# Performance work log

Measured on AMD Instinct MI355X. Metric: run time of the kernel, lower is better.

Reference implementation:

```python
import jax, jax.numpy as jnp
import numpy as np

B, N = 128, 128
FEAT_IN = 6   # feature_dim(4) + class + score
E = 32        # embedding_dim
NUM_CLASSES = 80


def setup_inputs() -> dict:
    key = jax.random.key(0)
    ks = jax.random.split(key, 20)
    def glorot(k, shape):
        fan_in, fan_out = shape[0], shape[1]
        lim = jnp.sqrt(6.0 / (fan_in + fan_out)).astype(jnp.float32)
        return jax.random.uniform(k, shape, jnp.float32, -lim, lim)
    return {
        'boxes': jax.random.uniform(ks[0], (B, N, 4), jnp.float32),
        'classes': jax.random.randint(ks[1], (B, N), 0, NUM_CLASSES),
        'scores': jax.random.uniform(ks[2], (B, N), jnp.float32),
        'num_objects': jax.random.randint(ks[3], (B,), 1, N + 1),
        # feature_encoder: Linear(6->32), ReLU, Linear(32->32)
        'W1': glorot(ks[4], (FEAT_IN, E)), 'b1': jnp.zeros((E,), jnp.float32),
        'W2': glorot(ks[5], (E, E)),       'b2': jnp.zeros((E,), jnp.float32),
        # isObject: Linear(32->32), ReLU, Linear(32->1), Sigmoid
        'Wo1': glorot(ks[6], (E, E)),  'bo1': jnp.zeros((E,), jnp.float32),
        'Wo2': glorot(ks[7], (E, 1)),  'bo2': jnp.zeros((1,), jnp.float32),
        # sameClass: Linear(64->32), ReLU, Linear(32->1), Sigmoid
        'Ws1': glorot(ks[8], (2 * E, E)), 'bs1': jnp.zeros((E,), jnp.float32),
        'Ws2': glorot(ks[9], (E, 1)),     'bs2': jnp.zeros((1,), jnp.float32),
    }


def reference(boxes, classes, scores, num_objects, W1, b1, W2, b2,
              Wo1, bo1, Wo2, bo2, Ws1, bs1, Ws2, bs2):
    # encode: [B,N,6] -> [B,N,E]
    combined = jnp.concatenate(
        [boxes, classes.astype(jnp.float32)[..., None], scores[..., None]], axis=-1)
    enc = jax.nn.relu(combined @ W1 + b1) @ W2 + b2                 # [B,N,E]

    # isObject predicate -> [B,N]
    isobj = jax.nn.sigmoid(jax.nn.relu(enc @ Wo1 + bo1) @ Wo2 + bo2)[..., 0]

    # sameClass on all pairs: split concat-weight so we never build [B,N,N,2E]
    Wsx, Wsy = Ws1[:E], Ws1[E:]
    hx = enc @ Wsx                                                  # [B,N,E]
    hy = enc @ Wsy                                                  # [B,N,E]
    h = jax.nn.relu(hx[:, :, None, :] + hy[:, None, :, :] + bs1)    # [B,N,N,E]
    same = jax.nn.sigmoid(h @ Ws2 + bs2)[..., 0]                    # [B,N,N] (x,y)

    # inner = And_min(isObject(y), sameClass(x,y))
    inner = jnp.minimum(isobj[:, None, :], same)                    # [B,N,N]

    mask = jnp.arange(N)[None, :] < num_objects[:, None]            # [B,N] valid objs
    n = num_objects.astype(jnp.float32)
    denom = jnp.maximum(n, 1.0)

    # Exists_y = mean over valid y
    exists = jnp.sum(inner * mask[:, None, :], axis=-1) / denom[:, None]  # [B,N]

    # outer = Or_max(Not(isObject(x)), exists)
    outer = jnp.maximum(1.0 - isobj, exists)                        # [B,N]

    # Forall_x = min over valid x (pad with 1.0, never the min for valid batches)
    sat_b = jnp.min(jnp.where(mask, outer, 1.0), axis=-1)           # [B]

    valid = (num_objects > 0).astype(jnp.float32)
    cnt = jnp.sum(valid)
    total = jnp.where(cnt > 0,
                      jnp.sum(sat_b * valid) / jnp.maximum(cnt, 1.0),
                      jnp.float32(1.0))
    return total
```

## Files before the change

### kernel.cpp

```cpp
#include <hip/hip_runtime.h>

#define BB 128
#define NN 128
#define EE 32


__global__ __launch_bounds__(256) void ltn_fused(
    const float* __restrict__ boxes, const int* __restrict__ classes,
    const float* __restrict__ scores, const int* __restrict__ num_objects,
    const float* __restrict__ W1, const float* __restrict__ b1,
    const float* __restrict__ W2, const float* __restrict__ b2,
    const float* __restrict__ Wo1, const float* __restrict__ bo1,
    const float* __restrict__ Wo2, const float* __restrict__ bo2,
    const float* __restrict__ Ws1, const float* __restrict__ bs1,
    const float* __restrict__ Ws2, const float* __restrict__ bs2,
    float* __restrict__ ws)
{
    __shared__ float hyS[128 * 36];
    __shared__ float hxS[128 * 36];
    __shared__ float rows[16 * 36];
    __shared__ float isoS[128];
    __shared__ float wred[4];

    const int t = threadIdx.x;
    const int b = blockIdx.x >> 1;
    const int half = blockIdx.x & 1;
    const int e = t & 31;
    const int g = t >> 5;

    float w1c[6];
#pragma unroll
    for (int f = 0; f < 6; f++) w1c[f] = W1[f * 32 + e];
    float w2c[32], wo1c[32], wsxc[32], wsyc[32];
#pragma unroll
    for (int k = 0; k < 32; k++) {
        w2c[k]  = W2[k * 32 + e];
        wo1c[k] = Wo1[k * 32 + e];
        wsxc[k] = Ws1[k * 32 + e];
        wsyc[k] = Ws1[(32 + k) * 32 + e];
    }
    const float b1e  = b1[e];
    const float b2e  = b2[e];
    const float bo1e = bo1[e];
    const float wo2e = Wo2[e];
    const float bo2s = bo2[0];

    const int il0 = g * 16;
#pragma unroll 2
    for (int it = 0; it < 16; ++it) {
        const int il = il0 + it;
        const int item = b * 128 + il;
        float* row = rows + (g * 2 + (it & 1)) * 36;

        const float4 bx = ((const float4*)boxes)[item];
        const float c4 = (float)classes[item];
        const float c5 = scores[item];

        float h1 = b1e;
        h1 = fmaf(bx.x, w1c[0], h1);
        h1 = fmaf(bx.y, w1c[1], h1);
        h1 = fmaf(bx.z, w1c[2], h1);
        h1 = fmaf(bx.w, w1c[3], h1);
        h1 = fmaf(c4,   w1c[4], h1);
        h1 = fmaf(c5,   w1c[5], h1);
        h1 = fmaxf(h1, 0.f);

        row[e] = h1;

        float a0 = 0.f, a1 = 0.f, a2 = 0.f, a3 = 0.f;
#pragma unroll
        for (int kk = 0; kk < 8; kk++) {
            const float4 h = *(const float4*)(row + kk * 4);
            a0 = fmaf(h.x, w2c[4 * kk + 0], a0);
            a1 = fmaf(h.y, w2c[4 * kk + 1], a1);
            a2 = fmaf(h.z, w2c[4 * kk + 2], a2);
            a3 = fmaf(h.w, w2c[4 * kk + 3], a3);
        }
        const float enc = ((a0 + a1) + (a2 + a3)) + b2e;
        row[e] = enc;

        float u = bo1e, hx = 0.f, hy = 0.f;
#pragma unroll
        for (int kk = 0; kk < 8; kk++) {
            const float4 ec = *(const float4*)(row + kk * 4);
            const int k0 = 4 * kk;
            u  = fmaf(ec.x, wo1c[k0 + 0], u);
            u  = fmaf(ec.y, wo1c[k0 + 1], u);
            u  = fmaf(ec.z, wo1c[k0 + 2], u);
            u  = fmaf(ec.w, wo1c[k0 + 3], u);
            hx = fmaf(ec.x, wsxc[k0 + 0], hx);
            hx = fmaf(ec.y, wsxc[k0 + 1], hx);
            hx = fmaf(ec.z, wsxc[k0 + 2], hx);
            hx = fmaf(ec.w, wsxc[k0 + 3], hx);
            hy = fmaf(ec.x, wsyc[k0 + 0], hy);
            hy = fmaf(ec.y, wsyc[k0 + 1], hy);
            hy = fmaf(ec.z, wsyc[k0 + 2], hy);
            hy = fmaf(ec.w, wsyc[k0 + 3], hy);
        }
        u = fmaxf(u, 0.f);

        float v = u * wo2e;
        v += __shfl_xor(v, 16, 32);
        v += __shfl_xor(v, 8, 32);
        v += __shfl_xor(v, 4, 32);
        v += __shfl_xor(v, 2, 32);
        v += __shfl_xor(v, 1, 32);

        hyS[il * 36 + e] = hy;
        hxS[il * 36 + e] = hx;
        if (e == 0)
            isoS[il] = 1.f / (1.f + __expf(-(v + bo2s)));
    }
    __syncthreads();

    const int nb = num_objects[b];
    const int p  = t >> 3;
    const int li0 = half * 64 + p * 2;
    const int li1 = li0 + 1;
    const int s  = t & 7;

    float hxb0[32], hxb1[32];
#pragma unroll
    for (int kk = 0; kk < 8; kk++) {
        const float4 a = ((const float4*)(hxS + li0 * 36))[kk];
        const float4 c = ((const float4*)(hxS + li1 * 36))[kk];
        const int k0 = 4 * kk;
        hxb0[k0 + 0] = a.x + bs1[k0 + 0];  hxb1[k0 + 0] = c.x + bs1[k0 + 0];
        hxb0[k0 + 1] = a.y + bs1[k0 + 1];  hxb1[k0 + 1] = c.y + bs1[k0 + 1];
        hxb0[k0 + 2] = a.z + bs1[k0 + 2];  hxb1[k0 + 2] = c.z + bs1[k0 + 2];
        hxb0[k0 + 3] = a.w + bs1[k0 + 3];  hxb1[k0 + 3] = c.w + bs1[k0 + 3];
    }
    float w2[32];
#pragma unroll
    for (int k = 0; k < 32; k++) w2[k] = Ws2[k];
    const float bbias = bs2[0];

    float acc0 = 0.f, acc1 = 0.f;
    for (int j = s; j < nb; j += 8) {
        const float4* hr4 = (const float4*)(hyS + j * 36);
        float d0 = bbias, d1 = 0.f, d2 = 0.f, d3 = 0.f;
        float e0 = bbias, e1 = 0.f, e2 = 0.f, e3 = 0.f;
#pragma unroll
        for (int kk = 0; kk < 8; kk++) {
            const float4 h = hr4[kk];
            const int k0 = 4 * kk;
            d0 = fmaf(fmaxf(hxb0[k0 + 0] + h.x, 0.f), w2[k0 + 0], d0);
            d1 = fmaf(fmaxf(hxb0[k0 + 1] + h.y, 0.f), w2[k0 + 1], d1);
            d2 = fmaf(fmaxf(hxb0[k0 + 2] + h.z, 0.f), w2[k0 + 2], d2);
            d3 = fmaf(fmaxf(hxb0[k0 + 3] + h.w, 0.f), w2[k0 + 3], d3);
            e0 = fmaf(fmaxf(hxb1[k0 + 0] + h.x, 0.f), w2[k0 + 0], e0);
            e1 = fmaf(fmaxf(hxb1[k0 + 1] + h.y, 0.f), w2[k0 + 1], e1);
            e2 = fmaf(fmaxf(hxb1[k0 + 2] + h.z, 0.f), w2[k0 + 2], e2);
            e3 = fmaf(fmaxf(hxb1[k0 + 3] + h.w, 0.f), w2[k0 + 3], e3);
        }
        const float dd = (d0 + d1) + (d2 + d3);
        const float ee = (e0 + e1) + (e2 + e3);
        const float same0 = 1.f / (1.f + __expf(-dd));
        const float same1 = 1.f / (1.f + __expf(-ee));
        const float iso_j = isoS[j];
        acc0 += fminf(iso_j, same0);
        acc1 += fminf(iso_j, same1);
    }
    acc0 += __shfl_xor(acc0, 1);  acc1 += __shfl_xor(acc1, 1);
    acc0 += __shfl_xor(acc0, 2);  acc1 += __shfl_xor(acc1, 2);
    acc0 += __shfl_xor(acc0, 4);  acc1 += __shfl_xor(acc1, 4);

    const float denom = (float)(nb > 1 ? nb : 1);
    const float ex0 = acc0 / denom;
    const float ex1 = acc1 / denom;
    const float o0 = fmaxf(1.f - isoS[li0], ex0);
    const float o1 = fmaxf(1.f - isoS[li1], ex1);
    float val = fminf((li0 < nb) ? o0 : 1.f, (li1 < nb) ? o1 : 1.f);

    val = fminf(val, __shfl_xor(val, 8));
    val = fminf(val, __shfl_xor(val, 16));
    val = fminf(val, __shfl_xor(val, 32));
    if ((t & 63) == 0) wred[t >> 6] = val;
    __syncthreads();

    if (t == 0)
        ws[blockIdx.x] = fminf(fminf(wred[0], wred[1]), fminf(wred[2], wred[3]));
}

__global__ __launch_bounds__(128) void finalize_kernel(
    const int* __restrict__ num_objects, const float* __restrict__ ws,
    float* __restrict__ out)
{
    __shared__ float r1[2], r2[2];
    const int t = threadIdx.x;
    const float sat = fminf(ws[2 * t], ws[2 * t + 1]);
    const float valid = (num_objects[t] > 0) ? 1.f : 0.f;
    float contrib = sat * valid;
    float vcnt = valid;
#pragma unroll
    for (int off = 1; off < 64; off <<= 1) {
        contrib += __shfl_xor(contrib, off);
        vcnt    += __shfl_xor(vcnt, off);
    }
    if ((t & 63) == 0) { r1[t >> 6] = contrib; r2[t >> 6] = vcnt; }
    __syncthreads();
    if (t == 0) {
        const float sc = r1[0] + r1[1];
        const float cn = r2[0] + r2[1];
        out[0] = (cn > 0.f) ? (sc / cn) : 1.f;
    }
}

extern "C" void kernel_launch(void* const* d_in, const int* in_sizes, int n_in,
                              void* d_out, int out_size, void* d_ws, size_t ws_size,
                              hipStream_t stream)
{
    const float* boxes       = (const float*)d_in[0];
    const int*   classes     = (const int*)d_in[1];
    const float* scores      = (const float*)d_in[2];
    const int*   num_objects = (const int*)d_in[3];
    const float* W1  = (const float*)d_in[4];
    const float* b1  = (const float*)d_in[5];
    const float* W2  = (const float*)d_in[6];
    const float* b2  = (const float*)d_in[7];
    const float* Wo1 = (const float*)d_in[8];
    const float* bo1 = (const float*)d_in[9];
    const float* Wo2 = (const float*)d_in[10];
    const float* bo2 = (const float*)d_in[11];
    const float* Ws1 = (const float*)d_in[12];
    const float* bs1 = (const float*)d_in[13];
    const float* Ws2 = (const float*)d_in[14];
    const float* bs2 = (const float*)d_in[15];

    float* ws  = (float*)d_ws;
    float* out = (float*)d_out;

    ltn_fused<<<256, 256, 0, stream>>>(boxes, classes, scores, num_objects,
                                       W1, b1, W2, b2, Wo1, bo1, Wo2, bo2,
                                       Ws1, bs1, Ws2, bs2, ws);
    finalize_kernel<<<1, 128, 0, stream>>>(num_objects, ws, out);
}
```

Before: 104.4 us.

## Double block size to 512 threads, one x-row per thread group

Launches 512 threads per block instead of 256. The encoder stage now gives each 32-lane group 8 items instead of 16, and the pairwise stage gives each 8-thread group a single x row instead of two. This doubles the resident threads per block to hide latency and shortens the per-thread serial work. In exchange, each hy row loaded from shared memory is reused for only one x row, and the per-thread register budget is tighter under the 512-thread launch bound, because every thread still keeps about 128 weight values in registers.

```diff
diff --git a/kernel.cpp b/kernel.cpp
--- a/kernel.cpp
+++ b/kernel.cpp
@@ -5,7 +5,7 @@
 #define EE 32
 
 
-__global__ __launch_bounds__(256) void ltn_fused(
+__global__ __launch_bounds__(512) void ltn_fused(
     const float* __restrict__ boxes, const int* __restrict__ classes,
     const float* __restrict__ scores, const int* __restrict__ num_objects,
     const float* __restrict__ W1, const float* __restrict__ b1,
@@ -18,9 +18,9 @@
 {
     __shared__ float hyS[128 * 36];
     __shared__ float hxS[128 * 36];
-    __shared__ float rows[16 * 36];
+    __shared__ float rows[32 * 36];
     __shared__ float isoS[128];
-    __shared__ float wred[4];
+    __shared__ float wred[8];
 
     const int t = threadIdx.x;
     const int b = blockIdx.x >> 1;
@@ -45,9 +45,9 @@
     const float wo2e = Wo2[e];
     const float bo2s = bo2[0];
 
-    const int il0 = g * 16;
+    const int il0 = g * 8;
 #pragma unroll 2
-    for (int it = 0; it < 16; ++it) {
+    for (int it = 0; it < 8; ++it) {
         const int il = il0 + it;
         const int item = b * 128 + il;
         float* row = rows + (g * 2 + (it & 1)) * 36;
@@ -115,62 +115,49 @@
 
     const int nb = num_objects[b];
     const int p  = t >> 3;
-    const int li0 = half * 64 + p * 2;
-    const int li1 = li0 + 1;
+    const int li = half * 64 + p;
     const int s  = t & 7;
 
-    float hxb0[32], hxb1[32];
+    float hxb[32];
 #pragma unroll
     for (int kk = 0; kk < 8; kk++) {
-        const float4 a = ((const float4*)(hxS + li0 * 36))[kk];
-        const float4 c = ((const float4*)(hxS + li1 * 36))[kk];
+        const float4 a = ((const float4*)(hxS + li * 36))[kk];
         const int k0 = 4 * kk;
-        hxb0[k0 + 0] = a.x + bs1[k0 + 0];  hxb1[k0 + 0] = c.x + bs1[k0 + 0];
-        hxb0[k0 + 1] = a.y + bs1[k0 + 1];  hxb1[k0 + 1] = c.y + bs1[k0 + 1];
-        hxb0[k0 + 2] = a.z + bs1[k0 + 2];  hxb1[k0 + 2] = c.z + bs1[k0 + 2];
-        hxb0[k0 + 3] = a.w + bs1[k0 + 3];  hxb1[k0 + 3] = c.w + bs1[k0 + 3];
+        hxb[k0 + 0] = a.x + bs1[k0 + 0];
+        hxb[k0 + 1] = a.y + bs1[k0 + 1];
+        hxb[k0 + 2] = a.z + bs1[k0 + 2];
+        hxb[k0 + 3] = a.w + bs1[k0 + 3];
     }
     float w2[32];
 #pragma unroll
     for (int k = 0; k < 32; k++) w2[k] = Ws2[k];
     const float bbias = bs2[0];
 
-    float acc0 = 0.f, acc1 = 0.f;
+    float acc = 0.f;
     for (int j = s; j < nb; j += 8) {
         const float4* hr4 = (const float4*)(hyS + j * 36);
         float d0 = bbias, d1 = 0.f, d2 = 0.f, d3 = 0.f;
-        float e0 = bbias, e1 = 0.f, e2 = 0.f, e3 = 0.f;
 #pragma unroll
         for (int kk = 0; kk < 8; kk++) {
             const float4 h = hr4[kk];
             const int k0 = 4 * kk;
-            d0 = fmaf(fmaxf(hxb0[k0 + 0] + h.x, 0.f), w2[k0 + 0], d0);
-            d1 = fmaf(fmaxf(hxb0[k0 + 1] + h.y, 0.f), w2[k0 + 1], d1);
-            d2 = fmaf(fmaxf(hxb0[k0 + 2] + h.z, 0.f), w2[k0 + 2], d2);
-            d3 = fmaf(fmaxf(hxb0[k0 + 3] + h.w, 0.f), w2[k0 + 3], d3);
-            e0 = fmaf(fmaxf(hxb1[k0 + 0] + h.x, 0.f), w2[k0 + 0], e0);
-            e1 = fmaf(fmaxf(hxb1[k0 + 1] + h.y, 0.f), w2[k0 + 1], e1);
-            e2 = fmaf(fmaxf(hxb1[k0 + 2] + h.z, 0.f), w2[k0 + 2], e2);
-            e3 = fmaf(fmaxf(hxb1[k0 + 3] + h.w, 0.f), w2[k0 + 3], e3);
+            d0 = fmaf(fmaxf(hxb[k0 + 0] + h.x, 0.f), w2[k0 + 0], d0);
+            d1 = fmaf(fmaxf(hxb[k0 + 1] + h.y, 0.f), w2[k0 + 1], d1);
+            d2 = fmaf(fmaxf(hxb[k0 + 2] + h.z, 0.f), w2[k0 + 2], d2);
+            d3 = fmaf(fmaxf(hxb[k0 + 3] + h.w, 0.f), w2[k0 + 3], d3);
         }
         const float dd = (d0 + d1) + (d2 + d3);
-        const float ee = (e0 + e1) + (e2 + e3);
-        const float same0 = 1.f / (1.f + __expf(-dd));
-        const float same1 = 1.f / (1.f + __expf(-ee));
-        const float iso_j = isoS[j];
-        acc0 += fminf(iso_j, same0);
-        acc1 += fminf(iso_j, same1);
-    }
-    acc0 += __shfl_xor(acc0, 1);  acc1 += __shfl_xor(acc1, 1);
-    acc0 += __shfl_xor(acc0, 2);  acc1 += __shfl_xor(acc1, 2);
-    acc0 += __shfl_xor(acc0, 4);  acc1 += __shfl_xor(acc1, 4);
+        const float same = 1.f / (1.f + __expf(-dd));
+        acc += fminf(isoS[j], same);
+    }
+    acc += __shfl_xor(acc, 1);
+    acc += __shfl_xor(acc, 2);
+    acc += __shfl_xor(acc, 4);
 
     const float denom = (float)(nb > 1 ? nb : 1);
-    const float ex0 = acc0 / denom;
-    const float ex1 = acc1 / denom;
-    const float o0 = fmaxf(1.f - isoS[li0], ex0);
-    const float o1 = fmaxf(1.f - isoS[li1], ex1);
-    float val = fminf((li0 < nb) ? o0 : 1.f, (li1 < nb) ? o1 : 1.f);
+    const float exists = acc / denom;
+    const float outer = fmaxf(1.f - isoS[li], exists);
+    float val = (li < nb) ? outer : 1.f;
 
     val = fminf(val, __shfl_xor(val, 8));
     val = fminf(val, __shfl_xor(val, 16));
@@ -178,8 +165,12 @@
     if ((t & 63) == 0) wred[t >> 6] = val;
     __syncthreads();
 
-    if (t == 0)
-        ws[blockIdx.x] = fminf(fminf(wred[0], wred[1]), fminf(wred[2], wred[3]));
+    if (t == 0) {
+        float m = wred[0];
+#pragma unroll
+        for (int w = 1; w < 8; w++) m = fminf(m, wred[w]);
+        ws[blockIdx.x] = m;
+    }
 }
 
 __global__ __launch_bounds__(128) void finalize_kernel(
@@ -230,7 +221,7 @@
     float* ws  = (float*)d_ws;
     float* out = (float*)d_out;
 
-    ltn_fused<<<256, 256, 0, stream>>>(boxes, classes, scores, num_objects,
+    ltn_fused<<<256, 512, 0, stream>>>(boxes, classes, scores, num_objects,
                                        W1, b1, W2, b2, Wo1, bo1, Wo2, bo2,
                                        Ws1, bs1, Ws2, bs2, ws);
     finalize_kernel<<<1, 128, 0, stream>>>(num_objects, ws, out);
```

New measurement: 100.5 us. 3.7% less time.
